# Kernel tuning notes

Hardware: AMD Instinct MI355X
Metric: run time of the kernel (lower is better)

## Reference

```python
import jax, jax.numpy as jnp
import numpy as np

B, S, D = 8, 1024, 1024
H, DK = 16, 64  # num_heads, d_k; H*DK == D
NEG_INF = 1e29


def setup_inputs() -> dict:
    key = jax.random.key(0)
    ks = jax.random.split(key, 12)
    sc = 1.0 / np.sqrt(D)
    q = jax.random.normal(ks[0], (B, S, D), jnp.float32)
    k = jax.random.normal(ks[1], (B, S, D), jnp.float32)
    v = jax.random.normal(ks[2], (B, S, D), jnp.float32)
    # causal mask, broadcast per batch (mask==0 positions are masked out)
    mask = jnp.broadcast_to(jnp.tril(jnp.ones((S, S), jnp.int32)), (B, S, S))
    Wq = jax.random.normal(ks[3], (D, D), jnp.float32) * sc
    bq = jax.random.normal(ks[4], (D,), jnp.float32) * 0.01
    Wk = jax.random.normal(ks[5], (D, D), jnp.float32) * sc
    bk = jax.random.normal(ks[6], (D,), jnp.float32) * 0.01
    Wv = jax.random.normal(ks[7], (D, D), jnp.float32) * sc
    bv = jax.random.normal(ks[8], (D,), jnp.float32) * 0.01
    Wo = jax.random.normal(ks[9], (D, D), jnp.float32) * sc
    bo = jax.random.normal(ks[10], (D,), jnp.float32) * 0.01
    return {"q": q, "k": k, "v": v, "mask": mask,
            "Wq": Wq, "bq": bq, "Wk": Wk, "bk": bk,
            "Wv": Wv, "bv": bv, "Wo": Wo, "bo": bo}


def reference(q, k, v, mask, Wq, bq, Wk, bk, Wv, bv, Wo, bo):
    # Linear projections (torch Linear: x @ W.T + b)
    q1 = q @ Wq.T + bq
    k1 = k @ Wk.T + bk
    v1 = v @ Wv.T + bv
    # [B, S, D] -> [B, H, S, DK]
    def split_heads(x):
        return x.reshape(B, S, H, DK).transpose(0, 2, 1, 3)
    q3, k3, v3 = split_heads(q1), split_heads(k1), split_heads(v1)
    # scores [B, H, S, S]
    scores = jnp.einsum('bhqd,bhkd->bhqk', q3, k3) / jnp.sqrt(jnp.float32(DK))
    scores = jnp.where(mask[:, None, :, :] == 0, -NEG_INF, scores)
    probs = jax.nn.softmax(scores, axis=-1)
    attn = jnp.einsum('bhqk,bhkd->bhqd', probs, v3)  # [B, H, S, DK]
    out = attn.transpose(0, 2, 1, 3).reshape(B, S, D)
    return out @ Wo.T + bo
```

## Files before the change

### kernel.cpp

```cpp
#include <hip/hip_runtime.h>
#include <hip/hip_bf16.h>
#include <stdint.h>

constexpr int NB = 8;
constexpr int NS = 1024;
constexpr int ND = 1024;
constexpr int NH = 16;
constexpr int NDK = 64;
constexpr int NT = NS / 64;

typedef __bf16 bf16_t;
typedef __attribute__((ext_vector_type(8))) __bf16 bf16x8;
typedef __attribute__((ext_vector_type(4))) __bf16 bf16x4;
typedef __attribute__((ext_vector_type(4))) float f32x4;

#define GLL16(g, s) __builtin_amdgcn_global_load_lds( \
    (const __attribute__((address_space(1))) void*)(g), \
    (__attribute__((address_space(3))) void*)(s), 16, 0, 0)

__device__ __forceinline__ void cvt_body(const float* __restrict__ s,
                                         bf16_t* __restrict__ d, long n) {
  long i0 = (long)(blockIdx.x * blockDim.x + threadIdx.x) * 4;
  long step = (long)gridDim.x * blockDim.x * 4;
  for (long i = i0; i < n; i += step) {
    float4 f = *(const float4*)(s + i);
    bf16x4 o;
    o[0] = (bf16_t)f.x; o[1] = (bf16_t)f.y; o[2] = (bf16_t)f.z; o[3] = (bf16_t)f.w;
    *(bf16x4*)(d + i) = o;
  }
}

__global__ __launch_bounds__(256) void cvt3_kernel(const float* s0, bf16_t* d0,
                                                   const float* s1, bf16_t* d1,
                                                   const float* s2, bf16_t* d2, long n) {
  const float* s = blockIdx.y == 0 ? s0 : blockIdx.y == 1 ? s1 : s2;
  bf16_t* d = blockIdx.y == 0 ? d0 : blockIdx.y == 1 ? d1 : d2;
  cvt_body(s, d, n);
}

__global__ __launch_bounds__(256) void cvt4_kernel(const float* s0, bf16_t* d0,
                                                   const float* s1, bf16_t* d1,
                                                   const float* s2, bf16_t* d2,
                                                   const float* s3, bf16_t* d3, long n) {
  const float* s = blockIdx.y == 0 ? s0 : blockIdx.y == 1 ? s1 : blockIdx.y == 2 ? s2 : s3;
  bf16_t* d = blockIdx.y == 0 ? d0 : blockIdx.y == 1 ? d1 : blockIdx.y == 2 ? d2 : d3;
  cvt_body(s, d, n);
}

template<bool OUT_F32>
__device__ __forceinline__ void gemm_body(bf16_t* S,
                                          const bf16_t* __restrict__ A,
                                          const bf16_t* __restrict__ W,
                                          const float* __restrict__ bias,
                                          void* __restrict__ Cout,
                                          int M, int N, int K, int bx, int by) {
  const int tid = threadIdx.x;
  const int l = tid & 63, w = tid >> 6;
  const int wr = w >> 1, wc = w & 1;
  const int g = l >> 4, r = l & 15;
  const int m0 = by * 256, n0 = bx * 128;
  const int wbase = w * 512;

  auto stageA = [&](int q, int t, int it) {
    int idx = it * 512 + tid;
    int row = idx >> 3, c = (idx & 7) ^ (row & 7);
    GLL16(A + (size_t)(m0 + row) * K + (t << 6) + c * 8,
          S + q * 24576 + it * 4096 + wbase);
  };
  auto stageB = [&](int q, int t, int it) {
    int idx = it * 512 + tid;
    int row = idx >> 3, c = (idx & 7) ^ (row & 7);
    GLL16(W + (size_t)(n0 + row) * K + (t << 6) + c * 8,
          S + q * 24576 + 16384 + it * 4096 + wbase);
  };

  f32x4 acc[4][4] = {};
  const int NKT = K >> 6;

#pragma unroll
  for (int it = 0; it < 4; ++it) stageA(0, 0, it);
#pragma unroll
  for (int it = 0; it < 2; ++it) stageB(0, 0, it);
#pragma unroll
  for (int it = 0; it < 4; ++it) stageA(1, 1, it);
#pragma unroll
  for (int it = 0; it < 2; ++it) stageB(1, 1, it);

  int q = 0;
  for (int t = 0; t < NKT; ++t) {
    const bool pf = (t + 2 < NKT);
    int q2 = q + 2; if (q2 >= 3) q2 -= 3;

    if (t + 1 < NKT) asm volatile("s_waitcnt vmcnt(6)" ::: "memory");
    else             asm volatile("s_waitcnt vmcnt(0)" ::: "memory");
    __builtin_amdgcn_s_barrier();

    const bf16_t* a_ = S + q * 24576;
    const bf16_t* b_ = a_ + 16384;

#pragma unroll
    for (int kk = 0; kk < 2; ++kk) {
      bf16x8 af[4], bw[4];
#pragma unroll
      for (int m = 0; m < 4; ++m) {
        int row = wr * 64 + m * 16 + r;
        af[m] = *(const bf16x8*)(a_ + row * 64 + (((kk * 4 + g) ^ (row & 7)) << 3));
      }
#pragma unroll
      for (int n = 0; n < 4; ++n) {
        int row = wc * 64 + n * 16 + r;
        bw[n] = *(const bf16x8*)(b_ + row * 64 + (((kk * 4 + g) ^ (row & 7)) << 3));
      }
      if (pf) {
        if (kk == 0) { stageA(q2, t + 2, 0); stageA(q2, t + 2, 1); stageA(q2, t + 2, 2); }
        else         { stageA(q2, t + 2, 3); stageB(q2, t + 2, 0); stageB(q2, t + 2, 1); }
      }
      __builtin_amdgcn_s_barrier();
      __builtin_amdgcn_s_setprio(1);
#pragma unroll
      for (int m = 0; m < 4; ++m)
#pragma unroll
        for (int n = 0; n < 4; ++n)
          acc[m][n] = __builtin_amdgcn_mfma_f32_16x16x32_bf16(af[m], bw[n], acc[m][n], 0, 0, 0);
      __builtin_amdgcn_s_setprio(0);
      if (kk == 0) __builtin_amdgcn_s_barrier();
    }
    ++q; if (q >= 3) q -= 3;
  }

#pragma unroll
  for (int n = 0; n < 4; ++n) {
    int col = n0 + wc * 64 + n * 16 + r;
    float bv = bias[col];
#pragma unroll
    for (int m = 0; m < 4; ++m) {
      int row0 = m0 + wr * 64 + m * 16 + g * 4;
#pragma unroll
      for (int j = 0; j < 4; ++j) {
        float vv = acc[m][n][j] + bv;
        if (OUT_F32)
          ((float*)Cout)[(size_t)(row0 + j) * N + col] = vv;
        else
          ((bf16_t*)Cout)[(size_t)(row0 + j) * N + col] = (bf16_t)vv;
      }
    }
  }
}

__global__ __launch_bounds__(512, 2) void gemm_bt(const bf16_t* __restrict__ A,
                                                  const bf16_t* __restrict__ W,
                                                  const float* __restrict__ bias,
                                                  float* __restrict__ Cout,
                                                  int M, int N, int K) {
  __shared__ bf16_t S[3 * 24576];
  const int o = blockIdx.x;
  const int xcd = o & 7, s = o >> 3;
  const int bx = s & 7, u = s >> 3;
  const int by = xcd + 8 * u;
  gemm_body<true>(S, A, W, bias, (void*)Cout, M, N, K, bx, by);
}

__global__ __launch_bounds__(512, 2) void gemm_qkv(
    const bf16_t* A0, const bf16_t* W0, const float* b0, bf16_t* C0,
    const bf16_t* A1, const bf16_t* W1, const float* b1, bf16_t* C1,
    const bf16_t* A2, const bf16_t* W2, const float* b2, bf16_t* C2,
    int M, int N, int K) {
  __shared__ bf16_t S[3 * 24576];
  const int o = blockIdx.x;
  const int xcd = o & 7, s = o >> 3;
  const int bx = s & 7, u = s >> 3;
  const int zby = xcd + 8 * u;
  const int z = zby >> 5, by = zby & 31;
  const bf16_t* A = z == 0 ? A0 : z == 1 ? A1 : A2;
  const bf16_t* W = z == 0 ? W0 : z == 1 ? W1 : W2;
  const float* bb = z == 0 ? b0 : z == 1 ? b1 : b2;
  bf16_t* C = z == 0 ? C0 : z == 1 ? C1 : C2;
  gemm_body<false>(S, A, W, bb, (void*)C, M, N, K, bx, by);
}

__global__ __launch_bounds__(256, 4) void attn_kernel(const bf16_t* __restrict__ Q1,
                                                      const bf16_t* __restrict__ K1,
                                                      const bf16_t* __restrict__ V1,
                                                      bf16_t* __restrict__ attn) {
  __shared__ bf16_t Kt[2][64 * 64];
  __shared__ bf16_t Vt[2][64 * 64];
  __shared__ bf16_t Pl[4][16 * 64];

  const int tid = threadIdx.x;
  const int l = tid & 63, w = tid >> 6;
  const int g = l >> 4, r = l & 15;

  const int o = blockIdx.x;
  const int os = (o & 7) * 128 + (o >> 3);
  const int pair = os & 7, hb = os >> 3;
  const int h = hb & 15, b = hb >> 4;

  constexpr float SC = 0.18033688011112042f;

  for (int ph = 0; ph < 2; ++ph) {
    const int qt = ph ? (NT - 1 - pair) : pair;
    const int qrow_g = qt * 64 + w * 16 + r;

    const bf16_t* qptr = Q1 + ((size_t)b * NS + qrow_g) * ND + h * 64;
    bf16x8 qf0 = *(const bf16x8*)(qptr + g * 8);
    bf16x8 qf1 = *(const bf16x8*)(qptr + 32 + g * 8);
#pragma unroll
    for (int i = 0; i < 8; ++i) {
      qf0[i] = (bf16_t)((float)qf0[i] * SC);
      qf1[i] = (bf16_t)((float)qf1[i] * SC);
    }

    float mrun = -1e30f, lrun = 0.f;
    f32x4 oacc[4] = {};

    __syncthreads();

    bf16x8 vr0, vr1;
    {
#pragma unroll
      for (int it = 0; it < 2; ++it) {
        int idx = it * 256 + tid;
        int key = idx >> 3;
        int dkg = ((idx & 7) ^ (key & 7)) << 3;
        GLL16(K1 + ((size_t)b * NS + key) * ND + h * 64 + dkg,
              &Kt[0][(it * 256 + w * 64) * 8]);
      }
      vr0 = *(const bf16x8*)(V1 + ((size_t)b * NS + l) * ND + h * 64 + w * 8);
      vr1 = *(const bf16x8*)(V1 + ((size_t)b * NS + l) * ND + h * 64 + (4 + w) * 8);
    }

    for (int kt = 0; kt <= qt; ++kt) {
      const int p = kt & 1;
      const int k0 = kt * 64;

#pragma unroll
      for (int it = 0; it < 2; ++it) {
        int dkb = (it * 4 + w) * 8;
#pragma unroll
        for (int jj = 0; jj < 8; ++jj) {
          int dk = dkb + jj;
          int boff = dk * 128 + ((l * 2) ^ ((dk & 7) << 4));
          *(bf16_t*)((char*)Vt[p] + boff) = (it ? vr1 : vr0)[jj];
        }
      }
      __syncthreads();

      if (kt < qt) {
        const int k0n = k0 + 64;
#pragma unroll
        for (int it = 0; it < 2; ++it) {
          int idx = it * 256 + tid;
          int key = idx >> 3;
          int dkg = ((idx & 7) ^ (key & 7)) << 3;
          GLL16(K1 + ((size_t)b * NS + k0n + key) * ND + h * 64 + dkg,
                &Kt[p ^ 1][(it * 256 + w * 64) * 8]);
        }
        vr0 = *(const bf16x8*)(V1 + ((size_t)b * NS + k0n + l) * ND + h * 64 + w * 8);
        vr1 = *(const bf16x8*)(V1 + ((size_t)b * NS + k0n + l) * ND + h * 64 + (4 + w) * 8);
      }

      f32x4 sacc[4] = {};
      __builtin_amdgcn_s_setprio(1);
#pragma unroll
      for (int n = 0; n < 4; ++n) {
        int key = n * 16 + r;
#pragma unroll
        for (int kk = 0; kk < 2; ++kk) {
          int dk2 = kk * 32 + g * 8;
          int boff = key * 128 + ((dk2 * 2) ^ ((key & 7) << 4));
          bf16x8 kf = *(const bf16x8*)((char*)Kt[p] + boff);
          sacc[n] = __builtin_amdgcn_mfma_f32_16x16x32_bf16(kf, kk == 0 ? qf0 : qf1, sacc[n], 0, 0, 0);
        }
      }
      __builtin_amdgcn_s_setprio(0);

      if (kt == qt) {
#pragma unroll
        for (int n = 0; n < 4; ++n)
#pragma unroll
          for (int j = 0; j < 4; ++j)
            if (k0 + n * 16 + g * 4 + j > qrow_g) sacc[n][j] = -1e30f;
      }

      float mx;
      {
        float t0 = fmaxf(fmaxf(sacc[0][0], sacc[0][1]), fmaxf(sacc[0][2], sacc[0][3]));
        float t1 = fmaxf(fmaxf(sacc[1][0], sacc[1][1]), fmaxf(sacc[1][2], sacc[1][3]));
        float t2 = fmaxf(fmaxf(sacc[2][0], sacc[2][1]), fmaxf(sacc[2][2], sacc[2][3]));
        float t3 = fmaxf(fmaxf(sacc[3][0], sacc[3][1]), fmaxf(sacc[3][2], sacc[3][3]));
        mx = fmaxf(fmaxf(t0, t1), fmaxf(t2, t3));
      }
      mx = fmaxf(mx, __shfl_xor(mx, 16));
      mx = fmaxf(mx, __shfl_xor(mx, 32));

      if (!__all(mx <= mrun + 8.0f)) {
        float m_new = fmaxf(mrun, mx);
        float esc = __builtin_amdgcn_exp2f(mrun - m_new);
        mrun = m_new;
        lrun *= esc;
#pragma unroll
        for (int n = 0; n < 4; ++n)
#pragma unroll
          for (int j = 0; j < 4; ++j) oacc[n][j] *= esc;
      }

      float rsum = 0.f;
#pragma unroll
      for (int n = 0; n < 4; ++n) {
        bf16x4 p4;
#pragma unroll
        for (int j = 0; j < 4; ++j) {
          float pe = __builtin_amdgcn_exp2f(sacc[n][j] - mrun);
          rsum += pe;
          p4[j] = (bf16_t)pe;
        }
        *(bf16x4*)((char*)Pl[w] + r * 128 + ((n * 32 + g * 8) ^ ((r & 7) << 4))) = p4;
      }
      rsum += __shfl_xor(rsum, 16);
      rsum += __shfl_xor(rsum, 32);
      lrun += rsum;

      __builtin_amdgcn_s_setprio(1);
#pragma unroll
      for (int kk = 0; kk < 2; ++kk) {
        bf16x8 pf = *(const bf16x8*)((char*)Pl[w] + r * 128 + ((kk * 64 + g * 16) ^ ((r & 7) << 4)));
#pragma unroll
        for (int n = 0; n < 4; ++n) {
          int dkr = n * 16 + r;
          bf16x8 vf = *(const bf16x8*)((char*)Vt[p] + dkr * 128 + ((kk * 64 + g * 16) ^ ((r & 7) << 4)));
          oacc[n] = __builtin_amdgcn_mfma_f32_16x16x32_bf16(vf, pf, oacc[n], 0, 0, 0);
        }
      }
      __builtin_amdgcn_s_setprio(0);
    }

    float linv = 1.0f / lrun;
#pragma unroll
    for (int n = 0; n < 4; ++n) {
      bf16x4 o4;
#pragma unroll
      for (int j = 0; j < 4; ++j) o4[j] = (bf16_t)(oacc[n][j] * linv);
      *(bf16x4*)(attn + ((size_t)b * NS + qrow_g) * ND + h * 64 + n * 16 + g * 4) = o4;
    }
  }
}

extern "C" void kernel_launch(void* const* d_in, const int* in_sizes, int n_in,
                              void* d_out, int out_size, void* d_ws, size_t ws_size,
                              hipStream_t stream) {
  const float* q  = (const float*)d_in[0];
  const float* k  = (const float*)d_in[1];
  const float* v  = (const float*)d_in[2];
  const float* Wq = (const float*)d_in[4];
  const float* bq = (const float*)d_in[5];
  const float* Wk = (const float*)d_in[6];
  const float* bk = (const float*)d_in[7];
  const float* Wv = (const float*)d_in[8];
  const float* bv = (const float*)d_in[9];
  const float* Wo = (const float*)d_in[10];
  const float* bo = (const float*)d_in[11];
  float* out = (float*)d_out;

  const size_t NX = (size_t)NB * NS * ND;
  const size_t NW = (size_t)ND * ND;
  char* ws = (char*)d_ws;
  size_t off = 0;
  auto alloc = [&](size_t bytes) {
    char* p = ws + off;
    off += (bytes + 255) & ~(size_t)255;
    return p;
  };
  bf16_t* xq  = (bf16_t*)alloc(NX * 2);
  bf16_t* xk  = (bf16_t*)alloc(NX * 2);
  bf16_t* xv  = (bf16_t*)alloc(NX * 2);
  bf16_t* wqb = (bf16_t*)alloc(NW * 2);
  bf16_t* wkb = (bf16_t*)alloc(NW * 2);
  bf16_t* wvb = (bf16_t*)alloc(NW * 2);
  bf16_t* wob = (bf16_t*)alloc(NW * 2);
  bf16_t* q1  = (bf16_t*)alloc(NX * 2);
  bf16_t* k1  = (bf16_t*)alloc(NX * 2);
  bf16_t* v1  = (bf16_t*)alloc(NX * 2);
  bf16_t* at  = xq;

  dim3 blk(256);
  cvt3_kernel<<<dim3(1024, 3), blk, 0, stream>>>(q, xq, k, xk, v, xv, (long)NX);
  cvt4_kernel<<<dim3(128, 4), blk, 0, stream>>>(Wq, wqb, Wk, wkb, Wv, wvb, Wo, wob, (long)NW);

  gemm_qkv<<<dim3(768), dim3(512), 0, stream>>>(
      xq, wqb, bq, q1, xk, wkb, bk, k1, xv, wvb, bv, v1, NB * NS, ND, ND);

  attn_kernel<<<dim3((NT / 2) * NH * NB), blk, 0, stream>>>(q1, k1, v1, at);

  gemm_bt<<<dim3(256), dim3(512), 0, stream>>>(at, wob, bo, out, NB * NS, ND, ND);
}
```

Baseline: 157.2 us.

## Load GEMM A operand directly to registers and shrink tiles to 128x128

The GEMM kernels now read the A operand straight from global memory into registers, double-buffered across k-steps, and stage only the weight tile through LDS with a 3-stage ring. The block tile drops from 256x128 with 512 threads to 128x128 with 256 threads, doubling grid sizes and raising occupancy to 3 blocks per CU. The goal is to cut LDS traffic and barriers for A and improve latency hiding. In exchange, A loads lose LDS sharing across the two column waves, so each A row is fetched twice from global/L2, and register pressure rises.

```diff
diff --git a/kernel.cpp b/kernel.cpp
--- a/kernel.cpp
+++ b/kernel.cpp
@@ -8,6 +8,7 @@
 constexpr int NH = 16;
 constexpr int NDK = 64;
 constexpr int NT = NS / 64;
+constexpr int NKT = ND / 64;
 
 typedef __bf16 bf16_t;
 typedef __attribute__((ext_vector_type(8))) __bf16 bf16x8;
@@ -53,79 +54,78 @@
                                           const bf16_t* __restrict__ W,
                                           const float* __restrict__ bias,
                                           void* __restrict__ Cout,
-                                          int M, int N, int K, int bx, int by) {
+                                          int bx, int by) {
   const int tid = threadIdx.x;
   const int l = tid & 63, w = tid >> 6;
   const int wr = w >> 1, wc = w & 1;
   const int g = l >> 4, r = l & 15;
-  const int m0 = by * 256, n0 = bx * 128;
+  const int m0 = by * 128, n0 = bx * 128;
   const int wbase = w * 512;
 
-  auto stageA = [&](int q, int t, int it) {
-    int idx = it * 512 + tid;
-    int row = idx >> 3, c = (idx & 7) ^ (row & 7);
-    GLL16(A + (size_t)(m0 + row) * K + (t << 6) + c * 8,
-          S + q * 24576 + it * 4096 + wbase);
+  const bf16_t* abase = A + (size_t)(m0 + wr * 64 + r) * ND;
+
+  auto stageB = [&](int q, int t) {
+#pragma unroll
+    for (int it = 0; it < 4; ++it) {
+      int idx = it * 256 + tid;
+      int row = idx >> 3, c = (idx & 7) ^ (row & 7);
+      GLL16(W + (size_t)(n0 + row) * ND + (t << 6) + c * 8,
+            S + q * 8192 + it * 2048 + wbase);
+    }
   };
-  auto stageB = [&](int q, int t, int it) {
-    int idx = it * 512 + tid;
-    int row = idx >> 3, c = (idx & 7) ^ (row & 7);
-    GLL16(W + (size_t)(n0 + row) * K + (t << 6) + c * 8,
-          S + q * 24576 + 16384 + it * 4096 + wbase);
+
+  auto loadA = [&](bf16x8 (&dst)[8], int t) {
+#pragma unroll
+    for (int kk = 0; kk < 2; ++kk)
+#pragma unroll
+      for (int m = 0; m < 4; ++m)
+        dst[kk * 4 + m] = *(const bf16x8*)(abase + (size_t)m * 16 * ND + t * 64 + kk * 32 + g * 8);
   };
 
   f32x4 acc[4][4] = {};
-  const int NKT = K >> 6;
-
-#pragma unroll
-  for (int it = 0; it < 4; ++it) stageA(0, 0, it);
-#pragma unroll
-  for (int it = 0; it < 2; ++it) stageB(0, 0, it);
-#pragma unroll
-  for (int it = 0; it < 4; ++it) stageA(1, 1, it);
-#pragma unroll
-  for (int it = 0; it < 2; ++it) stageB(1, 1, it);
-
-  int q = 0;
-  for (int t = 0; t < NKT; ++t) {
-    const bool pf = (t + 2 < NKT);
+  bf16x8 aA[8], aB[8];
+
+  stageB(0, 0);
+  stageB(1, 1);
+  loadA(aA, 0);
+
+  auto body = [&](int t, int q, bf16x8 (&cur)[8], bf16x8 (&nxt)[8]) {
     int q2 = q + 2; if (q2 >= 3) q2 -= 3;
-
-    if (t + 1 < NKT) asm volatile("s_waitcnt vmcnt(6)" ::: "memory");
-    else             asm volatile("s_waitcnt vmcnt(0)" ::: "memory");
+    if (t + 1 < NKT) loadA(nxt, t + 1);
+    __builtin_amdgcn_sched_barrier(0);
+    if (t + 2 < NKT) stageB(q2, t + 2);
+    __builtin_amdgcn_sched_barrier(0);
+    if (t + 2 < NKT)      asm volatile("s_waitcnt vmcnt(16)" ::: "memory");
+    else if (t + 1 < NKT) asm volatile("s_waitcnt vmcnt(12)" ::: "memory");
+    else                  asm volatile("s_waitcnt vmcnt(0)" ::: "memory");
     __builtin_amdgcn_s_barrier();
 
-    const bf16_t* a_ = S + q * 24576;
-    const bf16_t* b_ = a_ + 16384;
-
+    const bf16_t* b_ = S + q * 8192;
 #pragma unroll
     for (int kk = 0; kk < 2; ++kk) {
-      bf16x8 af[4], bw[4];
-#pragma unroll
-      for (int m = 0; m < 4; ++m) {
-        int row = wr * 64 + m * 16 + r;
-        af[m] = *(const bf16x8*)(a_ + row * 64 + (((kk * 4 + g) ^ (row & 7)) << 3));
-      }
+      bf16x8 bw[4];
 #pragma unroll
       for (int n = 0; n < 4; ++n) {
         int row = wc * 64 + n * 16 + r;
         bw[n] = *(const bf16x8*)(b_ + row * 64 + (((kk * 4 + g) ^ (row & 7)) << 3));
       }
-      if (pf) {
-        if (kk == 0) { stageA(q2, t + 2, 0); stageA(q2, t + 2, 1); stageA(q2, t + 2, 2); }
-        else         { stageA(q2, t + 2, 3); stageB(q2, t + 2, 0); stageB(q2, t + 2, 1); }
-      }
-      __builtin_amdgcn_s_barrier();
       __builtin_amdgcn_s_setprio(1);
 #pragma unroll
       for (int m = 0; m < 4; ++m)
 #pragma unroll
         for (int n = 0; n < 4; ++n)
-          acc[m][n] = __builtin_amdgcn_mfma_f32_16x16x32_bf16(af[m], bw[n], acc[m][n], 0, 0, 0);
+          acc[m][n] = __builtin_amdgcn_mfma_f32_16x16x32_bf16(cur[kk * 4 + m], bw[n], acc[m][n], 0, 0, 0);
       __builtin_amdgcn_s_setprio(0);
-      if (kk == 0) __builtin_amdgcn_s_barrier();
-    }
-    ++q; if (q >= 3) q -= 3;
+    }
+    asm volatile("s_waitcnt lgkmcnt(0)" ::: "memory");
+    __builtin_amdgcn_s_barrier();
+  };
+
+  int q = 0;
+#pragma unroll 1
+  for (int tt = 0; tt < NKT; tt += 2) {
+    body(tt, q, aA, aB);     ++q; if (q >= 3) q -= 3;
+    body(tt + 1, q, aB, aA); ++q; if (q >= 3) q -= 3;
   }
 
 #pragma unroll
@@ -139,43 +139,41 @@
       for (int j = 0; j < 4; ++j) {
         float vv = acc[m][n][j] + bv;
         if (OUT_F32)
-          ((float*)Cout)[(size_t)(row0 + j) * N + col] = vv;
+          ((float*)Cout)[(size_t)(row0 + j) * ND + col] = vv;
         else
-          ((bf16_t*)Cout)[(size_t)(row0 + j) * N + col] = (bf16_t)vv;
+          ((bf16_t*)Cout)[(size_t)(row0 + j) * ND + col] = (bf16_t)vv;
       }
     }
   }
 }
 
-__global__ __launch_bounds__(512, 2) void gemm_bt(const bf16_t* __restrict__ A,
+__global__ __launch_bounds__(256, 3) void gemm_bt(const bf16_t* __restrict__ A,
                                                   const bf16_t* __restrict__ W,
                                                   const float* __restrict__ bias,
-                                                  float* __restrict__ Cout,
-                                                  int M, int N, int K) {
-  __shared__ bf16_t S[3 * 24576];
+                                                  float* __restrict__ Cout) {
+  __shared__ bf16_t S[3 * 8192];
   const int o = blockIdx.x;
   const int xcd = o & 7, s = o >> 3;
   const int bx = s & 7, u = s >> 3;
   const int by = xcd + 8 * u;
-  gemm_body<true>(S, A, W, bias, (void*)Cout, M, N, K, bx, by);
-}
-
-__global__ __launch_bounds__(512, 2) void gemm_qkv(
+  gemm_body<true>(S, A, W, bias, (void*)Cout, bx, by);
+}
+
+__global__ __launch_bounds__(256, 3) void gemm_qkv(
     const bf16_t* A0, const bf16_t* W0, const float* b0, bf16_t* C0,
     const bf16_t* A1, const bf16_t* W1, const float* b1, bf16_t* C1,
-    const bf16_t* A2, const bf16_t* W2, const float* b2, bf16_t* C2,
-    int M, int N, int K) {
-  __shared__ bf16_t S[3 * 24576];
+    const bf16_t* A2, const bf16_t* W2, const float* b2, bf16_t* C2) {
+  __shared__ bf16_t S[3 * 8192];
   const int o = blockIdx.x;
   const int xcd = o & 7, s = o >> 3;
   const int bx = s & 7, u = s >> 3;
   const int zby = xcd + 8 * u;
-  const int z = zby >> 5, by = zby & 31;
+  const int z = zby >> 6, by = zby & 63;
   const bf16_t* A = z == 0 ? A0 : z == 1 ? A1 : A2;
   const bf16_t* W = z == 0 ? W0 : z == 1 ? W1 : W2;
   const float* bb = z == 0 ? b0 : z == 1 ? b1 : b2;
   bf16_t* C = z == 0 ? C0 : z == 1 ? C1 : C2;
-  gemm_body<false>(S, A, W, bb, (void*)C, M, N, K, bx, by);
+  gemm_body<false>(S, A, W, bb, (void*)C, bx, by);
 }
 
 __global__ __launch_bounds__(256, 4) void attn_kernel(const bf16_t* __restrict__ Q1,
@@ -386,10 +384,10 @@
   cvt3_kernel<<<dim3(1024, 3), blk, 0, stream>>>(q, xq, k, xk, v, xv, (long)NX);
   cvt4_kernel<<<dim3(128, 4), blk, 0, stream>>>(Wq, wqb, Wk, wkb, Wv, wvb, Wo, wob, (long)NW);
 
-  gemm_qkv<<<dim3(768), dim3(512), 0, stream>>>(
-      xq, wqb, bq, q1, xk, wkb, bk, k1, xv, wvb, bv, v1, NB * NS, ND, ND);
+  gemm_qkv<<<dim3(1536), blk, 0, stream>>>(
+      xq, wqb, bq, q1, xk, wkb, bk, k1, xv, wvb, bv, v1);
 
   attn_kernel<<<dim3((NT / 2) * NH * NB), blk, 0, stream>>>(q1, k1, v1, at);
 
-  gemm_bt<<<dim3(256), dim3(512), 0, stream>>>(at, wob, bo, out, NB * NS, ND, ND);
-}
+  gemm_bt<<<dim3(512), blk, 0, stream>>>(at, wob, bo, out);
+}
```

After: 329.4 us. 110% more time.

## Split GEMM k-step into four phases interleaving LDS reads, prefetch, and MFMA

Applied to the files above, without the earlier changes.

Restructures the projection GEMM inner loop so each 64-wide k-tile is processed in four phases of two A fragments times four B fragments. Each phase issues its share of the global-to-LDS prefetch, waits on LDS reads, and runs MFMAs under raised priority with sched_barriers fencing the compiler. This is meant to interleave memory and matrix work more finely and cut register pressure from A fragments. In exchange it adds more barriers per k-tile and removes the kk==0 trailing barrier, which could raise sync overhead or change the hazard ordering.

```diff
diff --git a/kernel.cpp b/kernel.cpp
--- a/kernel.cpp
+++ b/kernel.cpp
@@ -61,30 +61,30 @@
   const int m0 = by * 256, n0 = bx * 128;
   const int wbase = w * 512;
 
-  auto stageA = [&](int q, int t, int it) {
-    int idx = it * 512 + tid;
-    int row = idx >> 3, c = (idx & 7) ^ (row & 7);
-    GLL16(A + (size_t)(m0 + row) * K + (t << 6) + c * 8,
-          S + q * 24576 + it * 4096 + wbase);
+  auto stageA2 = [&](int q, int t, int half) {
+#pragma unroll
+    for (int it = half * 2; it < half * 2 + 2; ++it) {
+      int idx = it * 512 + tid;
+      int row = idx >> 3, c = (idx & 7) ^ (row & 7);
+      GLL16(A + (size_t)(m0 + row) * K + (t << 6) + c * 8,
+            S + q * 24576 + it * 4096 + wbase);
+    }
   };
-  auto stageB = [&](int q, int t, int it) {
-    int idx = it * 512 + tid;
-    int row = idx >> 3, c = (idx & 7) ^ (row & 7);
-    GLL16(W + (size_t)(n0 + row) * K + (t << 6) + c * 8,
-          S + q * 24576 + 16384 + it * 4096 + wbase);
+  auto stageB2 = [&](int q, int t) {
+#pragma unroll
+    for (int it = 0; it < 2; ++it) {
+      int idx = it * 512 + tid;
+      int row = idx >> 3, c = (idx & 7) ^ (row & 7);
+      GLL16(W + (size_t)(n0 + row) * K + (t << 6) + c * 8,
+            S + q * 24576 + 16384 + it * 4096 + wbase);
+    }
   };
 
   f32x4 acc[4][4] = {};
   const int NKT = K >> 6;
 
-#pragma unroll
-  for (int it = 0; it < 4; ++it) stageA(0, 0, it);
-#pragma unroll
-  for (int it = 0; it < 2; ++it) stageB(0, 0, it);
-#pragma unroll
-  for (int it = 0; it < 4; ++it) stageA(1, 1, it);
-#pragma unroll
-  for (int it = 0; it < 2; ++it) stageB(1, 1, it);
+  stageA2(0, 0, 0); stageA2(0, 0, 1); stageB2(0, 0);
+  stageA2(1, 1, 0); stageA2(1, 1, 1); stageB2(1, 1);
 
   int q = 0;
   for (int t = 0; t < NKT; ++t) {
@@ -100,30 +100,39 @@
 
 #pragma unroll
     for (int kk = 0; kk < 2; ++kk) {
-      bf16x8 af[4], bw[4];
-#pragma unroll
-      for (int m = 0; m < 4; ++m) {
-        int row = wr * 64 + m * 16 + r;
-        af[m] = *(const bf16x8*)(a_ + row * 64 + (((kk * 4 + g) ^ (row & 7)) << 3));
-      }
+      bf16x8 bw[4];
 #pragma unroll
       for (int n = 0; n < 4; ++n) {
         int row = wc * 64 + n * 16 + r;
         bw[n] = *(const bf16x8*)(b_ + row * 64 + (((kk * 4 + g) ^ (row & 7)) << 3));
       }
-      if (pf) {
-        if (kk == 0) { stageA(q2, t + 2, 0); stageA(q2, t + 2, 1); stageA(q2, t + 2, 2); }
-        else         { stageA(q2, t + 2, 3); stageB(q2, t + 2, 0); stageB(q2, t + 2, 1); }
-      }
-      __builtin_amdgcn_s_barrier();
-      __builtin_amdgcn_s_setprio(1);
-#pragma unroll
-      for (int m = 0; m < 4; ++m)
-#pragma unroll
-        for (int n = 0; n < 4; ++n)
-          acc[m][n] = __builtin_amdgcn_mfma_f32_16x16x32_bf16(af[m], bw[n], acc[m][n], 0, 0, 0);
-      __builtin_amdgcn_s_setprio(0);
-      if (kk == 0) __builtin_amdgcn_s_barrier();
+#pragma unroll
+      for (int mh = 0; mh < 2; ++mh) {
+        bf16x8 af[2];
+#pragma unroll
+        for (int i = 0; i < 2; ++i) {
+          int row = wr * 64 + (mh * 2 + i) * 16 + r;
+          af[i] = *(const bf16x8*)(a_ + row * 64 + (((kk * 4 + g) ^ (row & 7)) << 3));
+        }
+        if (pf) {
+          int ph = kk * 2 + mh;
+          if (ph == 0)      stageA2(q2, t + 2, 0);
+          else if (ph == 1) stageA2(q2, t + 2, 1);
+          else if (ph == 2) stageB2(q2, t + 2);
+        }
+        __builtin_amdgcn_s_barrier();
+        asm volatile("s_waitcnt lgkmcnt(0)" ::: "memory");
+        __builtin_amdgcn_sched_barrier(0);
+        __builtin_amdgcn_s_setprio(1);
+#pragma unroll
+        for (int i = 0; i < 2; ++i)
+#pragma unroll
+          for (int n = 0; n < 4; ++n)
+            acc[mh * 2 + i][n] = __builtin_amdgcn_mfma_f32_16x16x32_bf16(
+                af[i], bw[n], acc[mh * 2 + i][n], 0, 0, 0);
+        __builtin_amdgcn_s_setprio(0);
+        __builtin_amdgcn_sched_barrier(0);
+      }
     }
     ++q; if (q >= 3) q -= 3;
   }
```

New measurement: 158.3 us. About the same (+0.7%).
